# Performance work log

Hardware: AMD Instinct MI355X
Metric: run time of the kernel (lower is better)

Reference implementation:

```python
import jax, jax.numpy as jnp
import numpy as np

N_NODES = 100000
N_EDGES = 1250000
D = 64


def setup_inputs() -> dict:
    key = jax.random.key(0)
    k1, k2, k3, k4 = jax.random.split(key, 4)
    x = jax.random.normal(k1, (N_NODES, D), dtype=jnp.float32)
    edge_index = jax.random.randint(k2, (2, N_EDGES), 0, N_NODES, dtype=jnp.int32)
    W1 = jax.random.normal(k3, (D, D), dtype=jnp.float32) * (1.0 / np.sqrt(D))
    b1 = jnp.zeros((D,), dtype=jnp.float32)
    W2 = jax.random.normal(k4, (D, D), dtype=jnp.float32) * (1.0 / np.sqrt(D))
    b2 = jnp.zeros((D,), dtype=jnp.float32)
    return {"x": x, "edge_index": edge_index, "W1": W1, "b1": b1, "W2": W2, "b2": b2}


def _gcn_conv(x, W, b, src, dst, norm):
    # PyG GCNConv: linear transform first, then normalized neighbor aggregation
    h = x @ W                                      # [N, D]
    msgs = h[src] * norm[:, None]                  # [E+N, D] gather + scale
    out = jax.ops.segment_sum(msgs, dst, num_segments=x.shape[0])  # scatter-add
    return out + b


def reference(x, edge_index, W1, b1, W2, b2):
    n = x.shape[0]
    # add self-loops
    loops = jnp.arange(n, dtype=edge_index.dtype)
    src = jnp.concatenate([edge_index[0], loops])
    dst = jnp.concatenate([edge_index[1], loops])
    # symmetric normalization D^{-1/2} (A+I) D^{-1/2}
    deg = jax.ops.segment_sum(jnp.ones_like(dst, dtype=x.dtype), dst, num_segments=n)
    dis = jnp.where(deg > 0, jax.lax.rsqrt(deg), 0.0)
    norm = dis[src] * dis[dst]

    identity = x
    h = jax.nn.relu(_gcn_conv(x, W1, b1, src, dst, norm))   # dropout = identity (eval)
    h = jax.nn.relu(_gcn_conv(h, W2, b2, src, dst, norm))
    return h + identity
```

## Files before the change

kernel.cpp:

```cpp
#include <hip/hip_runtime.h>

#define DFEAT 64
#define BSHIFT 7
#define BNODES 128
#define MAXB 1024
#define EPB 4096
#define XPAD 68

typedef unsigned int uint32;
typedef unsigned short ushort16;

__device__ __forceinline__ ushort16 f2bf(float f) {
    uint32 u = __float_as_uint(f);
    u += 0x7fffu + ((u >> 16) & 1u);
    return (ushort16)(u >> 16);
}
__device__ __forceinline__ float bf_lo(uint32 u) { return __uint_as_float(u << 16); }
__device__ __forceinline__ float bf_hi(uint32 u) { return __uint_as_float(u & 0xffff0000u); }

__global__ __launch_bounds__(256) void k_p1(
    const int* __restrict__ dst, int E, int* __restrict__ hist, int nblk, int nb) {
    __shared__ int h[MAXB];
    for (int i = threadIdx.x; i < nb; i += 256) h[i] = 0;
    __syncthreads();
    int base = blockIdx.x * EPB;
    int lim = E - base; if (lim > EPB) lim = EPB;
    for (int j = threadIdx.x; j < lim; j += 256)
        atomicAdd(&h[dst[base + j] >> BSHIFT], 1);
    __syncthreads();
    for (int i = threadIdx.x; i < nb; i += 256)
        hist[(size_t)i * nblk + blockIdx.x] = h[i];
}

__global__ __launch_bounds__(256) void k_p2a(
    const int* __restrict__ hist, int nblk, int nb, int* __restrict__ btot) {
    int w = (blockIdx.x * 256 + threadIdx.x) >> 6;
    int lane = threadIdx.x & 63;
    if (w >= nb) return;
    size_t base = (size_t)w * nblk;
    int s = 0;
    for (int k = lane; k < nblk; k += 64) s += hist[base + k];
#pragma unroll
    for (int d = 1; d < 64; d <<= 1) s += __shfl_xor(s, d, 64);
    if (lane == 0) btot[w] = s;
}

__global__ __launch_bounds__(256) void k_p2b(
    const int* __restrict__ btot, int nb, int* __restrict__ bstart) {
    __shared__ int lds[256];
    __shared__ int pre[257];
    int t = threadIdx.x;
    int c0 = t * 4;
    int v[4]; int s = 0;
#pragma unroll
    for (int j = 0; j < 4; ++j) { v[j] = (c0 + j < nb) ? btot[c0 + j] : 0; s += v[j]; }
    lds[t] = s; __syncthreads();
    if (t == 0) { int run = 0; for (int i = 0; i < 256; ++i) { pre[i] = run; run += lds[i]; } pre[256] = run; }
    __syncthreads();
    int run = pre[t];
#pragma unroll
    for (int j = 0; j < 4; ++j) {
        if (c0 + j < nb) bstart[c0 + j] = run;
        run += v[j];
    }
    if (t == 0) bstart[nb] = pre[256];
}

__global__ __launch_bounds__(256) void k_p2c(
    int* __restrict__ hist, int nblk, int nb, const int* __restrict__ bstart) {
    int w = (blockIdx.x * 256 + threadIdx.x) >> 6;
    int lane = threadIdx.x & 63;
    if (w >= nb) return;
    size_t base = (size_t)w * nblk;
    int run = bstart[w];
    for (int c = 0; c < nblk; c += 64) {
        int k = c + lane;
        int v = (k < nblk) ? hist[base + k] : 0;
        int sc = v;
#pragma unroll
        for (int d = 1; d < 64; d <<= 1) { int t = __shfl_up(sc, d, 64); if (lane >= d) sc += t; }
        if (k < nblk) hist[base + k] = run + sc - v;
        run += __shfl(sc, 63, 64);
    }
}

__global__ __launch_bounds__(256) void k_p3(
    const int* __restrict__ src, const int* __restrict__ dst, int E,
    const int* __restrict__ hist, int nblk, int nb, uint32* __restrict__ part) {
    __shared__ int cur[MAXB];
    for (int i = threadIdx.x; i < nb; i += 256) cur[i] = hist[(size_t)i * nblk + blockIdx.x];
    __syncthreads();
    int base = blockIdx.x * EPB;
    int lim = E - base; if (lim > EPB) lim = EPB;
    for (int j = threadIdx.x; j < lim; j += 256) {
        int d = dst[base + j];
        int s = src[base + j];
        int b = d >> BSHIFT;
        int pos = atomicAdd(&cur[b], 1);
        part[pos] = (uint32)s | ((uint32)(d & (BNODES - 1)) << 17);
    }
}

__global__ __launch_bounds__(256) void k_sort(
    const uint32* __restrict__ part, const int* __restrict__ bstart,
    int* __restrict__ row_ptr, int* __restrict__ col, float* __restrict__ dis,
    int n, int nb) {
    __shared__ int cnt[BNODES];
    __shared__ int off[BNODES + 1];
    int b = blockIdx.x;
    int node0 = b << BSHIFT;
    int nn = n - node0; if (nn > BNODES) nn = BNODES;

    if (threadIdx.x < BNODES) cnt[threadIdx.x] = 0;
    __syncthreads();
    int beg = bstart[b], end = bstart[b + 1];
    for (int i = beg + threadIdx.x; i < end; i += 256)
        atomicAdd(&cnt[part[i] >> 17], 1);
    __syncthreads();
    if (threadIdx.x == 0) {
        int run = beg;
        for (int j = 0; j < BNODES; ++j) { off[j] = run; run += cnt[j]; }
        off[BNODES] = run;
    }
    __syncthreads();
    if (threadIdx.x < nn) {
        row_ptr[node0 + threadIdx.x] = off[threadIdx.x];
        dis[node0 + threadIdx.x] = rsqrtf((float)cnt[threadIdx.x] + 1.0f);
    }
    if (b == nb - 1 && threadIdx.x == 0) row_ptr[n] = end;
    if (threadIdx.x < BNODES) cnt[threadIdx.x] = 0;
    __syncthreads();
    for (int i = beg + threadIdx.x; i < end; i += 256) {
        uint32 p = part[i];
        int j = p >> 17;
        int pos = off[j] + atomicAdd(&cnt[j], 1);
        col[pos] = (int)(p & 0x1FFFFu);
    }
}

__global__ __launch_bounds__(256) void k_gemm_scale(
    const float* __restrict__ X, const float* __restrict__ W,
    const float* __restrict__ dis, ushort16* __restrict__ gb, int n) {
    __shared__ float Ws[64 * 64];
    __shared__ float Xs[64 * XPAD];

    {
        float4* Wv = (float4*)Ws;
        const float4* Wg = (const float4*)W;
        for (int i = threadIdx.x; i < 64 * 16; i += 256) Wv[i] = Wg[i];
    }
    int row0 = blockIdx.x * 64;
    int rows = n - row0; if (rows > 64) rows = 64;
    {
        const float4* Xg = (const float4*)(X + (size_t)row0 * 64);
        for (int i = threadIdx.x; i < rows * 16; i += 256) {
            int row = i >> 4, c = i & 15;
            ((float4*)(Xs + row * XPAD))[c] = Xg[i];
        }
    }
    __syncthreads();

    int tj = threadIdx.x & 15;
    int ti = threadIdx.x >> 4;

    float acc[4][4];
#pragma unroll
    for (int r = 0; r < 4; ++r)
#pragma unroll
        for (int c = 0; c < 4; ++c) acc[r][c] = 0.f;

#pragma unroll 2
    for (int k4 = 0; k4 < 64; k4 += 4) {
        float4 w0 = *(const float4*)(Ws + (k4 + 0) * 64 + 4 * tj);
        float4 w1 = *(const float4*)(Ws + (k4 + 1) * 64 + 4 * tj);
        float4 w2 = *(const float4*)(Ws + (k4 + 2) * 64 + 4 * tj);
        float4 w3 = *(const float4*)(Ws + (k4 + 3) * 64 + 4 * tj);
#pragma unroll
        for (int r = 0; r < 4; ++r) {
            float4 xv = *(const float4*)(Xs + (4 * ti + r) * XPAD + k4);
            acc[r][0] = fmaf(xv.x, w0.x, acc[r][0]);
            acc[r][1] = fmaf(xv.x, w0.y, acc[r][1]);
            acc[r][2] = fmaf(xv.x, w0.z, acc[r][2]);
            acc[r][3] = fmaf(xv.x, w0.w, acc[r][3]);
            acc[r][0] = fmaf(xv.y, w1.x, acc[r][0]);
            acc[r][1] = fmaf(xv.y, w1.y, acc[r][1]);
            acc[r][2] = fmaf(xv.y, w1.z, acc[r][2]);
            acc[r][3] = fmaf(xv.y, w1.w, acc[r][3]);
            acc[r][0] = fmaf(xv.z, w2.x, acc[r][0]);
            acc[r][1] = fmaf(xv.z, w2.y, acc[r][1]);
            acc[r][2] = fmaf(xv.z, w2.z, acc[r][2]);
            acc[r][3] = fmaf(xv.z, w2.w, acc[r][3]);
            acc[r][0] = fmaf(xv.w, w3.x, acc[r][0]);
            acc[r][1] = fmaf(xv.w, w3.y, acc[r][1]);
            acc[r][2] = fmaf(xv.w, w3.z, acc[r][2]);
            acc[r][3] = fmaf(xv.w, w3.w, acc[r][3]);
        }
    }

#pragma unroll
    for (int r = 0; r < 4; ++r) {
        int row = 4 * ti + r;
        if (row < rows) {
            float dn = dis[row0 + row];
            ushort4 o;
            o.x = f2bf(acc[r][0] * dn);
            o.y = f2bf(acc[r][1] * dn);
            o.z = f2bf(acc[r][2] * dn);
            o.w = f2bf(acc[r][3] * dn);
            *(ushort4*)(gb + (size_t)(row0 + row) * 64 + 4 * tj) = o;
        }
    }
}

__global__ __launch_bounds__(256) void k_aggregate(
    const ushort16* __restrict__ gb, const int* __restrict__ row_ptr,
    const int* __restrict__ col, const float* __restrict__ dis,
    const float* __restrict__ bias, const float* __restrict__ resid,
    float* __restrict__ out, int n) {
    int node = blockIdx.x * 4 + (threadIdx.x >> 6);
    if (node >= n) return;
    int lane = threadIdx.x & 63;
    int slot = lane >> 3;
    int q    = lane & 7;
    const uint4* gq = (const uint4*)gb;

    int beg = row_ptr[node];
    int deg = row_ptr[node + 1] - beg;

    float acc[8];
#pragma unroll
    for (int j = 0; j < 8; ++j) acc[j] = 0.f;

    if (slot == 0) {
        uint4 u = gq[(uint32)node * 8u + (uint32)q];
        acc[0] += bf_lo(u.x); acc[1] += bf_hi(u.x);
        acc[2] += bf_lo(u.y); acc[3] += bf_hi(u.y);
        acc[4] += bf_lo(u.z); acc[5] += bf_hi(u.z);
        acc[6] += bf_lo(u.w); acc[7] += bf_hi(u.w);
    }

    for (int i = 0; i < deg; i += 16) {
        int v0 = i + slot;
        int v1 = i + 8 + slot;
        int m = deg - 1;
        int c0 = col[beg + (v0 < m ? v0 : m)];
        int c1 = col[beg + (v1 < m ? v1 : m)];
        uint4 u0 = gq[(uint32)c0 * 8u + (uint32)q];
        uint4 u1 = gq[(uint32)c1 * 8u + (uint32)q];
        float w0 = (v0 < deg) ? 1.f : 0.f;
        float w1 = (v1 < deg) ? 1.f : 0.f;
        acc[0] = fmaf(w0, bf_lo(u0.x), acc[0]); acc[1] = fmaf(w0, bf_hi(u0.x), acc[1]);
        acc[2] = fmaf(w0, bf_lo(u0.y), acc[2]); acc[3] = fmaf(w0, bf_hi(u0.y), acc[3]);
        acc[4] = fmaf(w0, bf_lo(u0.z), acc[4]); acc[5] = fmaf(w0, bf_hi(u0.z), acc[5]);
        acc[6] = fmaf(w0, bf_lo(u0.w), acc[6]); acc[7] = fmaf(w0, bf_hi(u0.w), acc[7]);
        acc[0] = fmaf(w1, bf_lo(u1.x), acc[0]); acc[1] = fmaf(w1, bf_hi(u1.x), acc[1]);
        acc[2] = fmaf(w1, bf_lo(u1.y), acc[2]); acc[3] = fmaf(w1, bf_hi(u1.y), acc[3]);
        acc[4] = fmaf(w1, bf_lo(u1.z), acc[4]); acc[5] = fmaf(w1, bf_hi(u1.z), acc[5]);
        acc[6] = fmaf(w1, bf_lo(u1.w), acc[6]); acc[7] = fmaf(w1, bf_hi(u1.w), acc[7]);
    }

#pragma unroll
    for (int j = 0; j < 8; ++j) {
        acc[j] += __shfl_xor(acc[j], 8, 64);
        acc[j] += __shfl_xor(acc[j], 16, 64);
        acc[j] += __shfl_xor(acc[j], 32, 64);
    }

    if (slot == 0) {
        float dn = dis[node];
        float r[8];
#pragma unroll
        for (int j = 0; j < 8; ++j)
            r[j] = fmaxf(fmaf(acc[j], dn, bias[q * 8 + j]), 0.f);
        if (resid) {
            const float4* rv = (const float4*)(resid + (size_t)node * DFEAT + q * 8);
            float4 x0 = rv[0], x1 = rv[1];
            r[0] += x0.x; r[1] += x0.y; r[2] += x0.z; r[3] += x0.w;
            r[4] += x1.x; r[5] += x1.y; r[6] += x1.z; r[7] += x1.w;
        }
        float4* ov = (float4*)(out + (size_t)node * DFEAT + q * 8);
        ov[0] = make_float4(r[0], r[1], r[2], r[3]);
        ov[1] = make_float4(r[4], r[5], r[6], r[7]);
    }
}


extern "C" void kernel_launch(void* const* d_in, const int* in_sizes, int n_in,
                              void* d_out, int out_size, void* d_ws, size_t ws_size,
                              hipStream_t stream) {
    const float* x  = (const float*)d_in[0];
    const int*   ei = (const int*)  d_in[1];
    const float* W1 = (const float*)d_in[2];
    const float* b1 = (const float*)d_in[3];
    const float* W2 = (const float*)d_in[4];
    const float* b2 = (const float*)d_in[5];
    float* out = (float*)d_out;

    const int n = in_sizes[0] / DFEAT;
    const int E = in_sizes[1] / 2;
    const int* src = ei;
    const int* dst = ei + E;

    const int nb   = (n + BNODES - 1) >> BSHIFT;
    const int nblk = (E + EPB - 1) / EPB;

    int*      hist    = (int*)d_ws;
    int*      btot    = hist + (((size_t)nb * nblk + 3) & ~3);
    int*      bstart  = btot + ((nb + 3) & ~3);
    uint32*   part    = (uint32*)(bstart + ((nb + 1 + 3) & ~3));
    int*      row_ptr = (int*)(part + ((E + 3) & ~3));
    int*      col     = row_ptr + ((n + 1 + 3) & ~3);
    float*    dis     = (float*)(col + ((E + 3) & ~3));
    ushort16* gb      = (ushort16*)(dis + ((n + 3) & ~3));
    float*    h       = (float*)(gb + (size_t)n * DFEAT);

    const int B256 = 256;
    const int gT   = (n + 63) / 64;
    const int gW   = ((nb * 64) + B256 - 1) / B256;
    const int gAg  = (n + 3) / 4;

    k_p1  <<<nblk, B256, 0, stream>>>(dst, E, hist, nblk, nb);
    k_p2a <<<gW,   B256, 0, stream>>>(hist, nblk, nb, btot);
    k_p2b <<<1,    B256, 0, stream>>>(btot, nb, bstart);
    k_p2c <<<gW,   B256, 0, stream>>>(hist, nblk, nb, bstart);
    k_p3  <<<nblk, B256, 0, stream>>>(src, dst, E, hist, nblk, nb, part);
    k_sort<<<nb,   B256, 0, stream>>>(part, bstart, row_ptr, col, dis, n, nb);

    k_gemm_scale<<<gT,  B256, 0, stream>>>(x, W1, dis, gb, n);
    k_aggregate <<<gAg, B256, 0, stream>>>(gb, row_ptr, col, dis, b1, nullptr, h, n);

    k_gemm_scale<<<gT,  B256, 0, stream>>>(h, W2, dis, gb, n);
    k_aggregate <<<gAg, B256, 0, stream>>>(gb, row_ptr, col, dis, b2, x, out, n);
}
```

Measured before the change: 239.7 us.

## Widen partition blocks, use wave-shuffle scans, add low-degree aggregate fast path

Raises the thread count of the histogram and scatter partition kernels from 256 to 1024 so each 4096-edge block finishes with fewer loop iterations. Replaces the serial single-thread prefix sums in the bucket-start and per-bucket offset computations with wavefront shuffle scans. Adds a single-load path in aggregation for nodes with degree of at most 8, skipping the second half-empty gather. This adds branch divergence between nodes with different degrees and changes occupancy for the partition kernels.

```diff
diff --git a/kernel.cpp b/kernel.cpp
--- a/kernel.cpp
+++ b/kernel.cpp
@@ -18,17 +18,17 @@
 __device__ __forceinline__ float bf_lo(uint32 u) { return __uint_as_float(u << 16); }
 __device__ __forceinline__ float bf_hi(uint32 u) { return __uint_as_float(u & 0xffff0000u); }
 
-__global__ __launch_bounds__(256) void k_p1(
+__global__ __launch_bounds__(1024) void k_p1(
     const int* __restrict__ dst, int E, int* __restrict__ hist, int nblk, int nb) {
     __shared__ int h[MAXB];
-    for (int i = threadIdx.x; i < nb; i += 256) h[i] = 0;
+    for (int i = threadIdx.x; i < nb; i += 1024) h[i] = 0;
     __syncthreads();
     int base = blockIdx.x * EPB;
     int lim = E - base; if (lim > EPB) lim = EPB;
-    for (int j = threadIdx.x; j < lim; j += 256)
+    for (int j = threadIdx.x; j < lim; j += 1024)
         atomicAdd(&h[dst[base + j] >> BSHIFT], 1);
     __syncthreads();
-    for (int i = threadIdx.x; i < nb; i += 256)
+    for (int i = threadIdx.x; i < nb; i += 1024)
         hist[(size_t)i * nblk + blockIdx.x] = h[i];
 }
 
@@ -47,23 +47,27 @@
 
 __global__ __launch_bounds__(256) void k_p2b(
     const int* __restrict__ btot, int nb, int* __restrict__ bstart) {
-    __shared__ int lds[256];
-    __shared__ int pre[257];
+    __shared__ int wsum[4];
     int t = threadIdx.x;
+    int lane = t & 63, w = t >> 6;
     int c0 = t * 4;
     int v[4]; int s = 0;
 #pragma unroll
     for (int j = 0; j < 4; ++j) { v[j] = (c0 + j < nb) ? btot[c0 + j] : 0; s += v[j]; }
-    lds[t] = s; __syncthreads();
-    if (t == 0) { int run = 0; for (int i = 0; i < 256; ++i) { pre[i] = run; run += lds[i]; } pre[256] = run; }
-    __syncthreads();
-    int run = pre[t];
+    int sc = s;
+#pragma unroll
+    for (int d = 1; d < 64; d <<= 1) { int tt = __shfl_up(sc, d, 64); if (lane >= d) sc += tt; }
+    if (lane == 63) wsum[w] = sc;
+    __syncthreads();
+    int base = 0;
+    for (int k = 0; k < w; ++k) base += wsum[k];
+    int run = base + sc - s;
 #pragma unroll
     for (int j = 0; j < 4; ++j) {
         if (c0 + j < nb) bstart[c0 + j] = run;
         run += v[j];
     }
-    if (t == 0) bstart[nb] = pre[256];
+    if (t == 255) bstart[nb] = base + sc;
 }
 
 __global__ __launch_bounds__(256) void k_p2c(
@@ -84,15 +88,15 @@
     }
 }
 
-__global__ __launch_bounds__(256) void k_p3(
+__global__ __launch_bounds__(1024) void k_p3(
     const int* __restrict__ src, const int* __restrict__ dst, int E,
     const int* __restrict__ hist, int nblk, int nb, uint32* __restrict__ part) {
     __shared__ int cur[MAXB];
-    for (int i = threadIdx.x; i < nb; i += 256) cur[i] = hist[(size_t)i * nblk + blockIdx.x];
+    for (int i = threadIdx.x; i < nb; i += 1024) cur[i] = hist[(size_t)i * nblk + blockIdx.x];
     __syncthreads();
     int base = blockIdx.x * EPB;
     int lim = E - base; if (lim > EPB) lim = EPB;
-    for (int j = threadIdx.x; j < lim; j += 256) {
+    for (int j = threadIdx.x; j < lim; j += 1024) {
         int d = dst[base + j];
         int s = src[base + j];
         int b = d >> BSHIFT;
@@ -117,10 +121,17 @@
     for (int i = beg + threadIdx.x; i < end; i += 256)
         atomicAdd(&cnt[part[i] >> 17], 1);
     __syncthreads();
-    if (threadIdx.x == 0) {
-        int run = beg;
-        for (int j = 0; j < BNODES; ++j) { off[j] = run; run += cnt[j]; }
-        off[BNODES] = run;
+    if (threadIdx.x < 64) {
+        int l = threadIdx.x;
+        int c0 = cnt[2 * l], c1 = cnt[2 * l + 1];
+        int s = c0 + c1;
+        int sc = s;
+#pragma unroll
+        for (int d = 1; d < 64; d <<= 1) { int tt = __shfl_up(sc, d, 64); if (l >= d) sc += tt; }
+        int ex = beg + sc - s;
+        off[2 * l] = ex;
+        off[2 * l + 1] = ex + c0;
+        if (l == 63) off[BNODES] = ex + s;
     }
     __syncthreads();
     if (threadIdx.x < nn) {
@@ -239,24 +250,35 @@
         acc[6] += bf_lo(u.w); acc[7] += bf_hi(u.w);
     }
 
-    for (int i = 0; i < deg; i += 16) {
-        int v0 = i + slot;
-        int v1 = i + 8 + slot;
+    if (deg > 0 && deg <= 8) {
         int m = deg - 1;
-        int c0 = col[beg + (v0 < m ? v0 : m)];
-        int c1 = col[beg + (v1 < m ? v1 : m)];
+        int c0 = col[beg + (slot < m ? slot : m)];
         uint4 u0 = gq[(uint32)c0 * 8u + (uint32)q];
-        uint4 u1 = gq[(uint32)c1 * 8u + (uint32)q];
-        float w0 = (v0 < deg) ? 1.f : 0.f;
-        float w1 = (v1 < deg) ? 1.f : 0.f;
+        float w0 = (slot < deg) ? 1.f : 0.f;
         acc[0] = fmaf(w0, bf_lo(u0.x), acc[0]); acc[1] = fmaf(w0, bf_hi(u0.x), acc[1]);
         acc[2] = fmaf(w0, bf_lo(u0.y), acc[2]); acc[3] = fmaf(w0, bf_hi(u0.y), acc[3]);
         acc[4] = fmaf(w0, bf_lo(u0.z), acc[4]); acc[5] = fmaf(w0, bf_hi(u0.z), acc[5]);
         acc[6] = fmaf(w0, bf_lo(u0.w), acc[6]); acc[7] = fmaf(w0, bf_hi(u0.w), acc[7]);
-        acc[0] = fmaf(w1, bf_lo(u1.x), acc[0]); acc[1] = fmaf(w1, bf_hi(u1.x), acc[1]);
-        acc[2] = fmaf(w1, bf_lo(u1.y), acc[2]); acc[3] = fmaf(w1, bf_hi(u1.y), acc[3]);
-        acc[4] = fmaf(w1, bf_lo(u1.z), acc[4]); acc[5] = fmaf(w1, bf_hi(u1.z), acc[5]);
-        acc[6] = fmaf(w1, bf_lo(u1.w), acc[6]); acc[7] = fmaf(w1, bf_hi(u1.w), acc[7]);
+    } else {
+        for (int i = 0; i < deg; i += 16) {
+            int v0 = i + slot;
+            int v1 = i + 8 + slot;
+            int m = deg - 1;
+            int c0 = col[beg + (v0 < m ? v0 : m)];
+            int c1 = col[beg + (v1 < m ? v1 : m)];
+            uint4 u0 = gq[(uint32)c0 * 8u + (uint32)q];
+            uint4 u1 = gq[(uint32)c1 * 8u + (uint32)q];
+            float w0 = (v0 < deg) ? 1.f : 0.f;
+            float w1 = (v1 < deg) ? 1.f : 0.f;
+            acc[0] = fmaf(w0, bf_lo(u0.x), acc[0]); acc[1] = fmaf(w0, bf_hi(u0.x), acc[1]);
+            acc[2] = fmaf(w0, bf_lo(u0.y), acc[2]); acc[3] = fmaf(w0, bf_hi(u0.y), acc[3]);
+            acc[4] = fmaf(w0, bf_lo(u0.z), acc[4]); acc[5] = fmaf(w0, bf_hi(u0.z), acc[5]);
+            acc[6] = fmaf(w0, bf_lo(u0.w), acc[6]); acc[7] = fmaf(w0, bf_hi(u0.w), acc[7]);
+            acc[0] = fmaf(w1, bf_lo(u1.x), acc[0]); acc[1] = fmaf(w1, bf_hi(u1.x), acc[1]);
+            acc[2] = fmaf(w1, bf_lo(u1.y), acc[2]); acc[3] = fmaf(w1, bf_hi(u1.y), acc[3]);
+            acc[4] = fmaf(w1, bf_lo(u1.z), acc[4]); acc[5] = fmaf(w1, bf_hi(u1.z), acc[5]);
+            acc[6] = fmaf(w1, bf_lo(u1.w), acc[6]); acc[7] = fmaf(w1, bf_hi(u1.w), acc[7]);
+        }
     }
 
 #pragma unroll
@@ -319,11 +341,11 @@
     const int gW   = ((nb * 64) + B256 - 1) / B256;
     const int gAg  = (n + 3) / 4;
 
-    k_p1  <<<nblk, B256, 0, stream>>>(dst, E, hist, nblk, nb);
+    k_p1  <<<nblk, 1024, 0, stream>>>(dst, E, hist, nblk, nb);
     k_p2a <<<gW,   B256, 0, stream>>>(hist, nblk, nb, btot);
     k_p2b <<<1,    B256, 0, stream>>>(btot, nb, bstart);
     k_p2c <<<gW,   B256, 0, stream>>>(hist, nblk, nb, bstart);
-    k_p3  <<<nblk, B256, 0, stream>>>(src, dst, E, hist, nblk, nb, part);
+    k_p3  <<<nblk, 1024, 0, stream>>>(src, dst, E, hist, nblk, nb, part);
     k_sort<<<nb,   B256, 0, stream>>>(part, bstart, row_ptr, col, dis, n, nb);
 
     k_gemm_scale<<<gT,  B256, 0, stream>>>(x, W1, dis, gb, n);
```

New measurement: 236.1 us. No clear change (-1.5%).
